# Kernel tuning notes

Hardware: AMD Instinct MI355X
Metric: run time of the kernel (lower is better)

## Reference

```python
import jax, jax.numpy as jnp
import numpy as np

N = 50000      # nodes (spots)
E = 800000     # edges (avg degree 16)
G = 1002       # num_genes + 2
D = 256        # latent_dim
C = 20         # num_celltypes
BN_EPS = 1e-5


def setup_inputs() -> dict:
    key = jax.random.key(0)
    ks = jax.random.split(key, 14)
    def p(k, shape, fan_in):
        return (jax.random.normal(k, shape, jnp.float32) / np.sqrt(fan_in)).astype(jnp.float32)
    return {
        "x": jax.random.normal(ks[0], (N, G), jnp.float32),
        "edge_index": jax.random.randint(ks[1], (2, E), 0, N, jnp.int64),
        "lin_w": p(ks[2], (G, D), G),          # encoder Linear (no bias)
        "conv1_w": p(ks[3], (D, D), D),
        "conv1_b": jnp.zeros((D,), jnp.float32),
        "conv2_w": p(ks[4], (D, D), D),
        "conv2_b": jnp.zeros((D,), jnp.float32),
        "mlp1_w": p(ks[5], (D, D), D),
        "mlp1_b": jnp.zeros((D,), jnp.float32),
        "bn_gamma": jnp.ones((D,), jnp.float32),
        "bn_beta": jnp.zeros((D,), jnp.float32),
        "mlp2_w": p(ks[6], (D, C), D),
        "mlp2_b": jnp.zeros((C,), jnp.float32),
    }


def _gcn_conv(x, src, dst, W, b):
    # x: [N, D]; symmetric GCN normalization with self-loops (weight 1)
    n = x.shape[0]
    x = x @ W
    deg = jax.ops.segment_sum(jnp.ones(src.shape[0], x.dtype), dst, num_segments=n) + 1.0
    dinv = jax.lax.rsqrt(deg)
    norm = dinv[src] * dinv[dst]                 # [E]
    agg = jax.ops.segment_sum(norm[:, None] * x[src], dst, num_segments=n)
    agg = agg + x * (1.0 / deg)[:, None]         # self-loop term: deg^-1 * x_i
    return agg + b


def reference(x, edge_index, lin_w, conv1_w, conv1_b, conv2_w, conv2_b,
              mlp1_w, mlp1_b, bn_gamma, bn_beta, mlp2_w, mlp2_b):
    src, dst = edge_index[0], edge_index[1]
    # encoder
    h = x @ lin_w
    h = jax.nn.relu(_gcn_conv(h, src, dst, conv1_w, conv1_b))
    h = jax.nn.relu(_gcn_conv(h, src, dst, conv2_w, conv2_b))
    # decoder MLP (Linear -> BatchNorm(train) -> ReLU -> Linear) + softmax
    h = h @ mlp1_w + mlp1_b
    mu = jnp.mean(h, axis=0)
    var = jnp.var(h, axis=0)
    h = (h - mu) * jax.lax.rsqrt(var + BN_EPS) * bn_gamma + bn_beta
    h = jax.nn.relu(h)
    h = h @ mlp2_w + mlp2_b
    return jax.nn.softmax(h, axis=-1)
```

## Files before the change

kernel.cpp:

```cpp
#include <hip/hip_runtime.h>
#include <cstdint>
#include <cstddef>

typedef unsigned short u16;
typedef unsigned int   u32;
typedef _Float16       f16;
typedef u16  u16x4 __attribute__((ext_vector_type(4)));
typedef u16  u16x8 __attribute__((ext_vector_type(8)));
typedef f16  f16x8 __attribute__((ext_vector_type(8)));
typedef float f32x4 __attribute__((ext_vector_type(4)));

static __device__ __forceinline__ u16 f2h(float f){
  f16 h = (f16)f;
  return __builtin_bit_cast(u16, h);
}
static __device__ __forceinline__ float h2f(u16 b){
  f16 h = __builtin_bit_cast(f16, b);
  return (float)h;
}

static __device__ __forceinline__ void async16(void* lds, const void* g){
  __builtin_amdgcn_global_load_lds(
      (const __attribute__((address_space(1))) u32*)g,
      (__attribute__((address_space(3))) u32*)lds, 16, 0, 0);
}

__global__ void transpose_weights(const float* __restrict__ w1, const float* __restrict__ w2,
                                  const float* __restrict__ w3,
                                  u16* __restrict__ w1T, u16* __restrict__ w2T,
                                  u16* __restrict__ w3T)
{
  __shared__ float t[32][33];
  int z = blockIdx.z;
  const float* in = (z==0)? w1 : (z==1)? w2 : w3;
  u16* out        = (z==0)? w1T: (z==1)? w2T: w3T;
  int by = blockIdx.y, bx = blockIdx.x;
  int tid = threadIdx.x;
  #pragma unroll
  for (int k=0;k<4;k++){
    int p = tid + k*256; int r = p>>5, c = p&31;
    t[r][c] = in[(by*32 + r)*256 + bx*32 + c];
  }
  __syncthreads();
  #pragma unroll
  for (int k=0;k<4;k++){
    int p = tid + k*256; int r = p>>5, c = p&31;
    out[(bx*32 + r)*256 + by*32 + c] = f2h(t[c][r]);
  }
}

__global__ __launch_bounds__(256) void cast_pad(
    const float* __restrict__ x, u16* __restrict__ xh, int N, int Npad, int G, int Gpad)
{
  int tid = threadIdx.x;
  int tpr = Gpad >> 3;
  int r   = blockIdx.x*(256/tpr) + tid/tpr;
  if (r >= Npad) return;
  int c0  = (tid % tpr) * 8;
  u16x8 o;
  if (r >= N){
    #pragma unroll
    for (int j=0;j<8;j++) o[j] = 0;
  } else {
    const float* xr = x + (size_t)r*G;
    if (c0 + 8 <= G){
      #pragma unroll
      for (int k=0;k<4;k++){
        float2 v = *(const float2*)(xr + c0 + k*2);
        o[k*2]   = f2h(v.x);
        o[k*2+1] = f2h(v.y);
      }
    } else {
      #pragma unroll
      for (int j=0;j<8;j++){
        int c = c0 + j;
        o[j] = (c < G) ? f2h(xr[c]) : (u16)0;
      }
    }
  }
  *(u16x8*)(xh + (size_t)r*Gpad + c0) = o;
}

__global__ void count_kernel(const int* __restrict__ dst, int* __restrict__ cnt, int E){
  int e = blockIdx.x*256 + threadIdx.x;
  if (e < E) atomicAdd(&cnt[dst[e]], 1);
}

__global__ void scan_reduce(const int* __restrict__ cnt, int* __restrict__ bsum, int N){
  __shared__ int s[256];
  int tid = threadIdx.x;
  int i = blockIdx.x*256 + tid;
  s[tid] = (i<N)? cnt[i] : 0;
  __syncthreads();
  for (int off=128; off>0; off>>=1){
    if (tid < off) s[tid] += s[tid+off];
    __syncthreads();
  }
  if (tid==0) bsum[blockIdx.x] = s[0];
}

__global__ void scan_offsets(const int* __restrict__ bsum, int* __restrict__ boff, int nb){
  __shared__ int s[256];
  int tid = threadIdx.x;
  int v = (tid<nb)? bsum[tid] : 0;
  s[tid] = v; __syncthreads();
  for (int off=1; off<256; off<<=1){
    int t = (tid>=off)? s[tid-off] : 0;
    __syncthreads();
    s[tid] += t;
    __syncthreads();
  }
  if (tid<nb) boff[tid] = s[tid]-v;
}

__global__ void scan_final(const int* __restrict__ cnt, const int* __restrict__ boff,
                           int* __restrict__ row_ptr, float* __restrict__ dinv, int N, int E){
  __shared__ int s[256];
  int tid = threadIdx.x;
  int i = blockIdx.x*256 + tid;
  int v = (i<N)? cnt[i] : 0;
  s[tid] = v; __syncthreads();
  for (int off=1; off<256; off<<=1){
    int t = (tid>=off)? s[tid-off] : 0;
    __syncthreads();
    s[tid] += t;
    __syncthreads();
  }
  if (i < N){
    row_ptr[i] = boff[blockIdx.x] + s[tid] - v;
    dinv[i] = rsqrtf((float)(v+1));
  }
  if (i == N-1) row_ptr[N] = E;
}

__global__ void scatter_kernel(const int* __restrict__ src, const int* __restrict__ dst,
                               const int* __restrict__ row_ptr, int* __restrict__ cursor,
                               int* __restrict__ colx, int E){
  int e = blockIdx.x*256 + threadIdx.x;
  if (e < E){
    int d = dst[e];
    int pos = atomicAdd(&cursor[d], 1);
    colx[row_ptr[d] + pos] = src[e];
  }
}

template<bool ADD_BIAS, bool STORE_T>
__global__ __launch_bounds__(256) void gemm_async(
    const u16* __restrict__ Ah,
    const u16* __restrict__ BT, int Kpad,
    u16* __restrict__ C, const float* __restrict__ bias, int M, int ldc)
{
  __shared__ __align__(16) u16 As[2][4096];
  __shared__ __align__(16) u16 Bs[2][4096];

  const int tid  = threadIdx.x;
  const int lane = tid & 63;
  const int quad = lane >> 4;
  const int l16  = lane & 15;
  const int wave = tid >> 6;
  const int wm = (wave >> 1) << 6;
  const int wn = (wave & 1) << 6;
  const int m0 = blockIdx.y << 7;
  const int n0 = blockIdx.x << 7;

  const u16* bg[2]; u16* lB[2];
  const u16* ag[2]; u16* lA[2];
  #pragma unroll
  for (int i=0;i<2;i++){
    int q = wave*2 + i;
    int rr = lane >> 2, ss = lane & 3;
    int gg = ss ^ ((rr >> 1) & 3);
    bg[i] = BT + (size_t)(n0 + q*16 + rr)*Kpad + gg*8;
    lB[i] = &Bs[0][0] + q*512;
    int gr = m0 + q*16 + rr;
    if (gr >= M) gr = M-1;
    ag[i] = Ah + (size_t)gr*Kpad + gg*8;
    lA[i] = &As[0][0] + q*512;
  }

  auto stage = [&](int buf, int t){
    const int kb = t << 5;
    #pragma unroll
    for (int i=0;i<2;i++) async16(lB[i] + buf*4096, bg[i] + kb);
    #pragma unroll
    for (int i=0;i<2;i++) async16(lA[i] + buf*4096, ag[i] + kb);
  };

  f32x4 acc[4][4];
  #pragma unroll
  for (int i=0;i<4;i++)
    #pragma unroll
    for (int j=0;j<4;j++) acc[i][j] = {0.f,0.f,0.f,0.f};

  const int NT = Kpad >> 5;

  stage(0, 0);
  int cur = 0;
  for (int t=0; t<NT; ++t){
    if (t+1 < NT){
      stage(cur^1, t+1);
      asm volatile("s_waitcnt vmcnt(4)" ::: "memory");
    } else {
      asm volatile("s_waitcnt vmcnt(0)" ::: "memory");
    }
    __builtin_amdgcn_s_barrier();

    const u16* AshC = &As[cur][0];
    const u16* BsC  = &Bs[cur][0];

    f16x8 af[4], bf[4];
    #pragma unroll
    for (int mt=0;mt<4;mt++){
      int R = wm + mt*16 + l16;
      int s = quad ^ ((R >> 1) & 3);
      af[mt] = __builtin_bit_cast(f16x8, *(const u16x8*)(AshC + R*32 + s*8));
    }
    #pragma unroll
    for (int nt=0;nt<4;nt++){
      int R = wn + nt*16 + l16;
      int s = quad ^ ((R >> 1) & 3);
      bf[nt] = __builtin_bit_cast(f16x8, *(const u16x8*)(BsC + R*32 + s*8));
    }
    #pragma unroll
    for (int mt=0;mt<4;mt++)
      #pragma unroll
      for (int nt=0;nt<4;nt++)
        acc[mt][nt] = __builtin_amdgcn_mfma_f32_16x16x32_f16(af[mt], bf[nt], acc[mt][nt], 0, 0, 0);

    __builtin_amdgcn_s_barrier();
    cur ^= 1;
  }

  if constexpr (STORE_T){
    #pragma unroll
    for (int mt=0;mt<4;mt++){
      #pragma unroll
      for (int nt=0;nt<4;nt++){
        int col  = n0 + wn + nt*16 + l16;
        int row0 = m0 + wm + mt*16 + quad*4;
        u16x4 o;
        #pragma unroll
        for (int r=0;r<4;r++) o[r] = f2h(acc[mt][nt][r]);
        if (row0 < M) *(u16x4*)(C + (size_t)col*ldc + row0) = o;
      }
    }
  } else {
    #pragma unroll
    for (int mt=0;mt<4;mt++){
      #pragma unroll
      for (int nt=0;nt<4;nt++){
        int col = n0 + wn + nt*16 + l16;
        float bv = 0.f;
        if constexpr (ADD_BIAS) bv = bias[col];
        #pragma unroll
        for (int r=0;r<4;r++){
          int row = m0 + wm + mt*16 + quad*4 + r;
          if (row < M) C[(size_t)row*256 + col] = f2h(acc[mt][nt][r] + bv);
        }
      }
    }
  }
}

__global__ __launch_bounds__(256) void agg_kernel(
    const u16* __restrict__ XW, const float* __restrict__ bias,
    const float* __restrict__ dinv, const int* __restrict__ row_ptr,
    const int* __restrict__ colx, u16* __restrict__ H, int N)
{
  int wid = (blockIdx.x << 2) + (threadIdx.x >> 6);
  if (wid >= N) return;
  int lane = threadIdx.x & 63;
  int f = lane << 2;
  float di = dinv[wid];
  int e0 = row_ptr[wid], e1 = row_ptr[wid+1];
  int deg = e1 - e0;
  float a0=0.f, a1=0.f, a2=0.f, a3=0.f;
  for (int base = 0; base < deg; base += 64){
    int mi = 0;
    if (base + lane < deg) mi = colx[e0 + base + lane];
    int cnt = min(deg - base, 64);
    int j = 0;
    for (; j+3 < cnt; j += 4){
      int s0 = __shfl(mi, j);
      int s1 = __shfl(mi, j+1);
      int s2 = __shfl(mi, j+2);
      int s3 = __shfl(mi, j+3);
      float w0 = dinv[s0]*di;
      float w1 = dinv[s1]*di;
      float w2 = dinv[s2]*di;
      float w3 = dinv[s3]*di;
      u16x4 x0 = *(const u16x4*)(XW + (size_t)s0*256 + f);
      u16x4 x1 = *(const u16x4*)(XW + (size_t)s1*256 + f);
      u16x4 x2 = *(const u16x4*)(XW + (size_t)s2*256 + f);
      u16x4 x3 = *(const u16x4*)(XW + (size_t)s3*256 + f);
      a0 += w0*h2f(x0[0]) + w1*h2f(x1[0]) + w2*h2f(x2[0]) + w3*h2f(x3[0]);
      a1 += w0*h2f(x0[1]) + w1*h2f(x1[1]) + w2*h2f(x2[1]) + w3*h2f(x3[1]);
      a2 += w0*h2f(x0[2]) + w1*h2f(x1[2]) + w2*h2f(x2[2]) + w3*h2f(x3[2]);
      a3 += w0*h2f(x0[3]) + w1*h2f(x1[3]) + w2*h2f(x2[3]) + w3*h2f(x3[3]);
    }
    for (; j < cnt; ++j){
      int s0 = __shfl(mi, j);
      float w0 = dinv[s0]*di;
      u16x4 x0 = *(const u16x4*)(XW + (size_t)s0*256 + f);
      a0 += w0*h2f(x0[0]); a1 += w0*h2f(x0[1]);
      a2 += w0*h2f(x0[2]); a3 += w0*h2f(x0[3]);
    }
  }
  u16x4 xs = *(const u16x4*)(XW + (size_t)wid*256 + f);
  float wd = di*di;
  a0 += wd*h2f(xs[0]); a1 += wd*h2f(xs[1]); a2 += wd*h2f(xs[2]); a3 += wd*h2f(xs[3]);
  const float4 bb = *(const float4*)(bias + f);
  a0 = fmaxf(a0 + bb.x, 0.f);
  a1 = fmaxf(a1 + bb.y, 0.f);
  a2 = fmaxf(a2 + bb.z, 0.f);
  a3 = fmaxf(a3 + bb.w, 0.f);
  u16x4 o = { f2h(a0), f2h(a1), f2h(a2), f2h(a3) };
  *(u16x4*)(H + (size_t)wid*256 + f) = o;
}

__global__ void bn_stats(const u16* __restrict__ H, float* __restrict__ bsum,
                         float* __restrict__ bsq, int N){
  int col = threadIdx.x;
  float s=0.f, q=0.f;
  for (int r=blockIdx.x; r<N; r+=gridDim.x){
    float v = h2f(H[(size_t)r*256 + col]);
    s += v; q += v*v;
  }
  atomicAdd(&bsum[col], s);
  atomicAdd(&bsq[col], q);
}

__global__ void bn_finalize(const float* __restrict__ bsum, const float* __restrict__ bsq,
                            const float* __restrict__ gamma, const float* __restrict__ beta,
                            float* __restrict__ scale, float* __restrict__ shift, int N){
  int c = threadIdx.x;
  float invN = 1.f/(float)N;
  float mu  = bsum[c]*invN;
  float var = bsq[c]*invN - mu*mu;
  float sc  = gamma[c] * rsqrtf(var + 1e-5f);
  scale[c] = sc;
  shift[c] = beta[c] - mu*sc;
}

__global__ __launch_bounds__(256) void final_kernel(
    const u16* __restrict__ H, const float* __restrict__ scale, const float* __restrict__ shift,
    const float* __restrict__ W2, const float* __restrict__ b2, float* __restrict__ out, int N)
{
  __shared__ float W2s[256*20];
  __shared__ float scs[256];
  __shared__ float shs[256];
  __shared__ float b2s[20];
  int tid = threadIdx.x;
  for (int i=tid; i<5120; i+=256) W2s[i] = W2[i];
  scs[tid] = scale[tid];
  shs[tid] = shift[tid];
  if (tid < 20) b2s[tid] = b2[tid];
  __syncthreads();
  int r = blockIdx.x*256 + tid;
  if (r >= N) return;
  float l[20];
  #pragma unroll
  for (int c=0;c<20;c++) l[c] = b2s[c];
  const u16* hrow = H + (size_t)r*256;
  for (int j0=0;j0<256;j0+=8){
    u16x8 h8 = *(const u16x8*)(hrow + j0);
    #pragma unroll
    for (int t=0;t<8;t++){
      int j = j0+t;
      float a = fmaxf(fmaf(h2f(h8[t]), scs[j], shs[j]), 0.f);
      const float* wr = W2s + j*20;
      #pragma unroll
      for (int c=0;c<20;c++) l[c] = fmaf(a, wr[c], l[c]);
    }
  }
  float m = l[0];
  #pragma unroll
  for (int c=1;c<20;c++) m = fmaxf(m, l[c]);
  float ssum = 0.f;
  #pragma unroll
  for (int c=0;c<20;c++){ l[c] = __expf(l[c]-m); ssum += l[c]; }
  float inv = 1.f/ssum;
  float* orow = out + (size_t)r*20;
  #pragma unroll
  for (int c=0;c<20;c++) orow[c] = l[c]*inv;
}

extern "C" void kernel_launch(void* const* d_in, const int* in_sizes, int n_in,
                              void* d_out, int out_size, void* d_ws, size_t ws_size,
                              hipStream_t stream)
{
  (void)n_in; (void)out_size; (void)ws_size;
  const float* x     = (const float*)d_in[0];
  const int*   ei    = (const int*)d_in[1];
  const float* lin_w = (const float*)d_in[2];
  const float* c1w   = (const float*)d_in[3];
  const float* c1b   = (const float*)d_in[4];
  const float* c2w   = (const float*)d_in[5];
  const float* c2b   = (const float*)d_in[6];
  const float* m1w   = (const float*)d_in[7];
  const float* m1b   = (const float*)d_in[8];
  const float* gam   = (const float*)d_in[9];
  const float* bet   = (const float*)d_in[10];
  const float* m2w   = (const float*)d_in[11];
  const float* m2b   = (const float*)d_in[12];
  float* out = (float*)d_out;

  const int E = in_sizes[1]/2;
  const int G = in_sizes[2]/256;
  const int N = in_sizes[0]/G;
  const int Gpad = (G + 31) & ~31;
  const int* srcI = ei;
  const int* dstI = ei + E;

  char* w = (char*)d_ws;
  auto alloc = [&](size_t bytes)->char*{
    char* p = w;
    w += (bytes + 255) & ~(size_t)255;
    return p;
  };
  u16* Ha    = (u16*)alloc((size_t)N*256*2);
  u16* Hb    = (u16*)alloc((size_t)N*256*2);
  u16* xh    = (u16*)alloc((size_t)N*Gpad*2);
  u16* linH  = (u16*)alloc((size_t)Gpad*256*2);
  u16* BT1   = (u16*)alloc((size_t)256*Gpad*2);
  u16* w1T   = (u16*)alloc(256*256*2);
  u16* w2T   = (u16*)alloc(256*256*2);
  u16* w3T   = (u16*)alloc(256*256*2);
  int* cnt    = (int*)alloc((size_t)N*4);
  int* cursor = (int*)alloc((size_t)N*4);
  int* rowp   = (int*)alloc((size_t)(N+1)*4);
  int* colx   = (int*)alloc((size_t)E*4);
  float* dinv = (float*)alloc((size_t)N*4);
  int* bsum   = (int*)alloc(1024);
  int* boff   = (int*)alloc(1024);
  float* bnsum= (float*)alloc(1024);
  float* bnsq = (float*)alloc(1024);
  float* scl  = (float*)alloc(1024);
  float* shf  = (float*)alloc(1024);

  hipMemsetAsync(cnt,    0, (size_t)N*4, stream);
  hipMemsetAsync(cursor, 0, (size_t)N*4, stream);
  hipMemsetAsync(bnsum,  0, 2048, stream);

  const int NB = (N + 255)/256;

  transpose_weights<<<dim3(8, 8, 3), 256, 0, stream>>>(c1w, c2w, m1w, w1T, w2T, w3T);
  cast_pad<<<dim3((Gpad+7)/8), 256, 0, stream>>>(lin_w, linH, G, Gpad, 256, 256);
  cast_pad<<<dim3((N+1)/2), 256, 0, stream>>>(x, xh, N, N, G, Gpad);
  gemm_async<false, true><<<dim3(2, Gpad/128), 256, 0, stream>>>(
      linH, w1T, 256, BT1, nullptr, Gpad, Gpad);

  count_kernel  <<<dim3((E+255)/256), 256, 0, stream>>>(dstI, cnt, E);
  scan_reduce   <<<dim3(NB), 256, 0, stream>>>(cnt, bsum, N);
  scan_offsets  <<<dim3(1),  256, 0, stream>>>(bsum, boff, NB);
  scan_final    <<<dim3(NB), 256, 0, stream>>>(cnt, boff, rowp, dinv, N, E);
  scatter_kernel<<<dim3((E+255)/256), 256, 0, stream>>>(srcI, dstI, rowp, cursor, colx, E);

  dim3 ggrid(2, (N+127)/128);
  gemm_async<false, false><<<ggrid, 256, 0, stream>>>(xh, BT1, Gpad, Hb, nullptr, N, 256);
  agg_kernel<<<dim3((N+3)/4), 256, 0, stream>>>(Hb, c1b, dinv, rowp, colx, Ha, N);
  gemm_async<false, false><<<ggrid, 256, 0, stream>>>(Ha, w2T, 256, Hb, nullptr, N, 256);
  agg_kernel<<<dim3((N+3)/4), 256, 0, stream>>>(Hb, c2b, dinv, rowp, colx, Ha, N);
  gemm_async<true, false><<<ggrid, 256, 0, stream>>>(Ha, w3T, 256, Hb, m1b, N, 256);
  bn_stats   <<<dim3(256), 256, 0, stream>>>(Hb, bnsum, bnsq, N);
  bn_finalize<<<dim3(1),   256, 0, stream>>>(bnsum, bnsq, gam, bet, scl, shf, N);
  final_kernel<<<dim3(NB), 256, 0, stream>>>(Hb, scl, shf, m2w, m2b, out, N);
}
```

Before: 706.9 us.

## Fuse BN statistics into GEMM epilogue and merge small prep kernels

Batch-norm sum and sum-of-squares are now computed in the last GEMM's epilogue with per-block LDS reduction and global atomics, which removes the separate bn_stats pass over H. bn_finalize is folded into final_kernel, the lin_w cast moves into the weight-prep kernel, and the two memsets are merged into one. Fewer launches and one less full read of H, at the cost of extra atomics and an epilogue barrier in the GEMM. Stats are taken from fp32 accumulators rather than the fp16-rounded H.

```diff
diff --git a/kernel.cpp b/kernel.cpp
--- a/kernel.cpp
+++ b/kernel.cpp
@@ -25,17 +25,44 @@
       (__attribute__((address_space(3))) u32*)lds, 16, 0, 0);
 }
 
-__global__ void transpose_weights(const float* __restrict__ w1, const float* __restrict__ w2,
-                                  const float* __restrict__ w3,
-                                  u16* __restrict__ w1T, u16* __restrict__ w2T,
-                                  u16* __restrict__ w3T)
+__global__ void prep_weights(const float* __restrict__ lw,
+                             const float* __restrict__ w1, const float* __restrict__ w2,
+                             const float* __restrict__ w3,
+                             u16* __restrict__ linH,
+                             u16* __restrict__ w1T, u16* __restrict__ w2T,
+                             u16* __restrict__ w3T, int G)
 {
+  int z = blockIdx.z;
+  int tid = threadIdx.x;
+  if (z == 3){
+    int bidx = blockIdx.y*8 + blockIdx.x;
+    int base = (bidx*256 + tid)*2;
+    #pragma unroll
+    for (int i=0;i<2;i++){
+      int p = base + i;
+      int row = p >> 5;
+      int c0  = (p & 31) * 8;
+      u16x8 o;
+      if (row < G){
+        const float* xr = lw + (size_t)row*256 + c0;
+        #pragma unroll
+        for (int k=0;k<4;k++){
+          float2 v = *(const float2*)(xr + k*2);
+          o[k*2]   = f2h(v.x);
+          o[k*2+1] = f2h(v.y);
+        }
+      } else {
+        #pragma unroll
+        for (int j=0;j<8;j++) o[j] = 0;
+      }
+      *(u16x8*)(linH + (size_t)row*256 + c0) = o;
+    }
+    return;
+  }
   __shared__ float t[32][33];
-  int z = blockIdx.z;
   const float* in = (z==0)? w1 : (z==1)? w2 : w3;
   u16* out        = (z==0)? w1T: (z==1)? w2T: w3T;
   int by = blockIdx.y, bx = blockIdx.x;
-  int tid = threadIdx.x;
   #pragma unroll
   for (int k=0;k<4;k++){
     int p = tid + k*256; int r = p>>5, c = p&31;
@@ -49,33 +76,27 @@
   }
 }
 
-__global__ __launch_bounds__(256) void cast_pad(
-    const float* __restrict__ x, u16* __restrict__ xh, int N, int Npad, int G, int Gpad)
+__global__ __launch_bounds__(256) void cast_x(
+    const float* __restrict__ x, u16* __restrict__ xh, int N, int G, int Gpad)
 {
   int tid = threadIdx.x;
-  int tpr = Gpad >> 3;
-  int r   = blockIdx.x*(256/tpr) + tid/tpr;
-  if (r >= Npad) return;
-  int c0  = (tid % tpr) * 8;
+  int r   = blockIdx.x*2 + (tid >> 7);
+  if (r >= N) return;
+  int c0  = (tid & 127) * 8;
+  const float* xr = x + (size_t)r*G;
   u16x8 o;
-  if (r >= N){
-    #pragma unroll
-    for (int j=0;j<8;j++) o[j] = 0;
+  if (c0 + 8 <= G){
+    #pragma unroll
+    for (int k=0;k<4;k++){
+      float2 v = *(const float2*)(xr + c0 + k*2);
+      o[k*2]   = f2h(v.x);
+      o[k*2+1] = f2h(v.y);
+    }
   } else {
-    const float* xr = x + (size_t)r*G;
-    if (c0 + 8 <= G){
-      #pragma unroll
-      for (int k=0;k<4;k++){
-        float2 v = *(const float2*)(xr + c0 + k*2);
-        o[k*2]   = f2h(v.x);
-        o[k*2+1] = f2h(v.y);
-      }
-    } else {
-      #pragma unroll
-      for (int j=0;j<8;j++){
-        int c = c0 + j;
-        o[j] = (c < G) ? f2h(xr[c]) : (u16)0;
-      }
+    #pragma unroll
+    for (int j=0;j<8;j++){
+      int c = c0 + j;
+      o[j] = (c < G) ? f2h(xr[c]) : (u16)0;
     }
   }
   *(u16x8*)(xh + (size_t)r*Gpad + c0) = o;
@@ -144,11 +165,12 @@
   }
 }
 
-template<bool ADD_BIAS, bool STORE_T>
+template<bool ADD_BIAS, bool STORE_T, bool STATS>
 __global__ __launch_bounds__(256) void gemm_async(
     const u16* __restrict__ Ah,
     const u16* __restrict__ BT, int Kpad,
-    u16* __restrict__ C, const float* __restrict__ bias, int M, int ldc)
+    u16* __restrict__ C, const float* __restrict__ bias, int M, int ldc,
+    float* __restrict__ bnsum, float* __restrict__ bnsq)
 {
   __shared__ __align__(16) u16 As[2][4096];
   __shared__ __align__(16) u16 Bs[2][4096];
@@ -231,6 +253,12 @@
     cur ^= 1;
   }
 
+  float bv[4] = {0.f, 0.f, 0.f, 0.f};
+  if constexpr (ADD_BIAS){
+    #pragma unroll
+    for (int nt=0;nt<4;nt++) bv[nt] = bias[n0 + wn + nt*16 + l16];
+  }
+
   if constexpr (STORE_T){
     #pragma unroll
     for (int mt=0;mt<4;mt++){
@@ -250,14 +278,42 @@
       #pragma unroll
       for (int nt=0;nt<4;nt++){
         int col = n0 + wn + nt*16 + l16;
-        float bv = 0.f;
-        if constexpr (ADD_BIAS) bv = bias[col];
         #pragma unroll
         for (int r=0;r<4;r++){
           int row = m0 + wm + mt*16 + quad*4 + r;
-          if (row < M) C[(size_t)row*256 + col] = f2h(acc[mt][nt][r] + bv);
+          if (row < M) C[(size_t)row*256 + col] = f2h(acc[mt][nt][r] + bv[nt]);
         }
       }
+    }
+  }
+
+  if constexpr (STATS){
+    float* ssum = (float*)&As[0][0];
+    float* ssq  = ssum + 128;
+    if (tid < 128){ ssum[tid] = 0.f; ssq[tid] = 0.f; }
+    __syncthreads();
+    #pragma unroll
+    for (int nt=0;nt<4;nt++){
+      float s = 0.f, q = 0.f;
+      #pragma unroll
+      for (int mt=0;mt<4;mt++){
+        #pragma unroll
+        for (int r=0;r<4;r++){
+          int row = m0 + wm + mt*16 + quad*4 + r;
+          if (row < M){
+            float v = acc[mt][nt][r] + bv[nt];
+            s += v; q += v*v;
+          }
+        }
+      }
+      int colL = wn + nt*16 + l16;
+      atomicAdd(&ssum[colL], s);
+      atomicAdd(&ssq[colL],  q);
+    }
+    __syncthreads();
+    if (tid < 128){
+      atomicAdd(&bnsum[n0 + tid], ssum[tid]);
+      atomicAdd(&bnsq[n0 + tid],  ssq[tid]);
     }
   }
 }
@@ -318,32 +374,10 @@
   *(u16x4*)(H + (size_t)wid*256 + f) = o;
 }
 
-__global__ void bn_stats(const u16* __restrict__ H, float* __restrict__ bsum,
-                         float* __restrict__ bsq, int N){
-  int col = threadIdx.x;
-  float s=0.f, q=0.f;
-  for (int r=blockIdx.x; r<N; r+=gridDim.x){
-    float v = h2f(H[(size_t)r*256 + col]);
-    s += v; q += v*v;
-  }
-  atomicAdd(&bsum[col], s);
-  atomicAdd(&bsq[col], q);
-}
-
-__global__ void bn_finalize(const float* __restrict__ bsum, const float* __restrict__ bsq,
-                            const float* __restrict__ gamma, const float* __restrict__ beta,
-                            float* __restrict__ scale, float* __restrict__ shift, int N){
-  int c = threadIdx.x;
-  float invN = 1.f/(float)N;
-  float mu  = bsum[c]*invN;
-  float var = bsq[c]*invN - mu*mu;
-  float sc  = gamma[c] * rsqrtf(var + 1e-5f);
-  scale[c] = sc;
-  shift[c] = beta[c] - mu*sc;
-}
-
 __global__ __launch_bounds__(256) void final_kernel(
-    const u16* __restrict__ H, const float* __restrict__ scale, const float* __restrict__ shift,
+    const u16* __restrict__ H,
+    const float* __restrict__ gamma, const float* __restrict__ beta,
+    const float* __restrict__ bnsum, const float* __restrict__ bnsq,
     const float* __restrict__ W2, const float* __restrict__ b2, float* __restrict__ out, int N)
 {
   __shared__ float W2s[256*20];
@@ -352,8 +386,14 @@
   __shared__ float b2s[20];
   int tid = threadIdx.x;
   for (int i=tid; i<5120; i+=256) W2s[i] = W2[i];
-  scs[tid] = scale[tid];
-  shs[tid] = shift[tid];
+  {
+    float invN = 1.f/(float)N;
+    float mu  = bnsum[tid]*invN;
+    float var = bnsq[tid]*invN - mu*mu;
+    float sc  = gamma[tid] * rsqrtf(var + 1e-5f);
+    scs[tid] = sc;
+    shs[tid] = beta[tid] - mu*sc;
+  }
   if (tid < 20) b2s[tid] = b2[tid];
   __syncthreads();
   int r = blockIdx.x*256 + tid;
@@ -426,8 +466,9 @@
   u16* w1T   = (u16*)alloc(256*256*2);
   u16* w2T   = (u16*)alloc(256*256*2);
   u16* w3T   = (u16*)alloc(256*256*2);
-  int* cnt    = (int*)alloc((size_t)N*4);
-  int* cursor = (int*)alloc((size_t)N*4);
+  const size_t szN = ((size_t)N*4 + 255) & ~(size_t)255;
+  int* cnt    = (int*)alloc(szN);
+  int* cursor = (int*)alloc(szN);
   int* rowp   = (int*)alloc((size_t)(N+1)*4);
   int* colx   = (int*)alloc((size_t)E*4);
   float* dinv = (float*)alloc((size_t)N*4);
@@ -435,20 +476,17 @@
   int* boff   = (int*)alloc(1024);
   float* bnsum= (float*)alloc(1024);
   float* bnsq = (float*)alloc(1024);
-  float* scl  = (float*)alloc(1024);
-  float* shf  = (float*)alloc(1024);
-
-  hipMemsetAsync(cnt,    0, (size_t)N*4, stream);
-  hipMemsetAsync(cursor, 0, (size_t)N*4, stream);
-  hipMemsetAsync(bnsum,  0, 2048, stream);
+
+  hipMemsetAsync(cnt,   0, szN*2, stream);
+  hipMemsetAsync(bnsum, 0, 2048, stream);
 
   const int NB = (N + 255)/256;
 
-  transpose_weights<<<dim3(8, 8, 3), 256, 0, stream>>>(c1w, c2w, m1w, w1T, w2T, w3T);
-  cast_pad<<<dim3((Gpad+7)/8), 256, 0, stream>>>(lin_w, linH, G, Gpad, 256, 256);
-  cast_pad<<<dim3((N+1)/2), 256, 0, stream>>>(x, xh, N, N, G, Gpad);
-  gemm_async<false, true><<<dim3(2, Gpad/128), 256, 0, stream>>>(
-      linH, w1T, 256, BT1, nullptr, Gpad, Gpad);
+  prep_weights<<<dim3(8, 8, 4), 256, 0, stream>>>(
+      lin_w, c1w, c2w, m1w, linH, w1T, w2T, w3T, G);
+  cast_x<<<dim3((N+1)/2), 256, 0, stream>>>(x, xh, N, G, Gpad);
+  gemm_async<false, true, false><<<dim3(2, Gpad/128), 256, 0, stream>>>(
+      linH, w1T, 256, BT1, nullptr, Gpad, Gpad, nullptr, nullptr);
 
   count_kernel  <<<dim3((E+255)/256), 256, 0, stream>>>(dstI, cnt, E);
   scan_reduce   <<<dim3(NB), 256, 0, stream>>>(cnt, bsum, N);
@@ -457,12 +495,13 @@
   scatter_kernel<<<dim3((E+255)/256), 256, 0, stream>>>(srcI, dstI, rowp, cursor, colx, E);
 
   dim3 ggrid(2, (N+127)/128);
-  gemm_async<false, false><<<ggrid, 256, 0, stream>>>(xh, BT1, Gpad, Hb, nullptr, N, 256);
+  gemm_async<false, false, false><<<ggrid, 256, 0, stream>>>(
+      xh, BT1, Gpad, Hb, nullptr, N, 256, nullptr, nullptr);
   agg_kernel<<<dim3((N+3)/4), 256, 0, stream>>>(Hb, c1b, dinv, rowp, colx, Ha, N);
-  gemm_async<false, false><<<ggrid, 256, 0, stream>>>(Ha, w2T, 256, Hb, nullptr, N, 256);
+  gemm_async<false, false, false><<<ggrid, 256, 0, stream>>>(
+      Ha, w2T, 256, Hb, nullptr, N, 256, nullptr, nullptr);
   agg_kernel<<<dim3((N+3)/4), 256, 0, stream>>>(Hb, c2b, dinv, rowp, colx, Ha, N);
-  gemm_async<true, false><<<ggrid, 256, 0, stream>>>(Ha, w3T, 256, Hb, m1b, N, 256);
-  bn_stats   <<<dim3(256), 256, 0, stream>>>(Hb, bnsum, bnsq, N);
-  bn_finalize<<<dim3(1),   256, 0, stream>>>(bnsum, bnsq, gam, bet, scl, shf, N);
-  final_kernel<<<dim3(NB), 256, 0, stream>>>(Hb, scl, shf, m2w, m2b, out, N);
-}
+  gemm_async<true, false, true><<<ggrid, 256, 0, stream>>>(
+      Ha, w3T, 256, Hb, m1b, N, 256, bnsum, bnsq);
+  final_kernel<<<dim3(NB), 256, 0, stream>>>(Hb, gam, bet, bnsum, bnsq, m2w, m2b, out, N);
+}
```

Result: faster. 649.5 us (-8.1%).
